# Kernel optimization log

Hardware: AMD Instinct MI355X
Metric: run time of the kernel (lower is better)

## Reference

```python
import jax, jax.numpy as jnp
import numpy as np

EMBED_DIM = 256
N_COMP = 50
SIGMA_INIT = 1.0
EPS = 1e-8


def setup_inputs() -> dict:
    key = jax.random.key(0)
    ks = jax.random.split(key, 9)
    B, N, D, C = 1, 8192, EMBED_DIM, N_COMP
    s = 0.05
    return {
        "embeddings": jax.random.normal(ks[0], (B, N, D), dtype=jnp.float32),
        # trajectory_projection: Linear(D, D//2) -> GELU -> (Dropout, eval) -> Linear(D//2, D//4) -> GELU -> Linear(D//4, C)
        "W1": jax.random.normal(ks[1], (D, D // 2), dtype=jnp.float32) * s,
        "b1": jnp.zeros((D // 2,), dtype=jnp.float32),
        "W2": jax.random.normal(ks[2], (D // 2, D // 4), dtype=jnp.float32) * s,
        "b2": jnp.zeros((D // 4,), dtype=jnp.float32),
        "W3": jax.random.normal(ks[3], (D // 4, C), dtype=jnp.float32) * s,
        "b3": jnp.zeros((C,), dtype=jnp.float32),
        "diffusion_weights": jax.random.normal(ks[4], (C,), dtype=jnp.float32),
        "adaptive_sigma": jnp.asarray(SIGMA_INIT, dtype=jnp.float32),
    }


def reference(embeddings, W1, b1, W2, b2, W3, b3, diffusion_weights, adaptive_sigma):
    B, N, D = embeddings.shape
    # trajectory projection (dropout is identity in eval mode); torch GELU default is exact (erf)
    h = jax.nn.gelu(embeddings @ W1 + b1, approximate=False)
    h = jax.nn.gelu(h @ W2 + b2, approximate=False)
    coords = h @ W3 + b3  # [B, N, C]

    # gaussian kernel: pairwise squared distances via sum-of-squares GEMM trick
    sq = jnp.sum(coords * coords, axis=-1)  # [B, N]
    d2 = sq[:, :, None] + sq[:, None, :] - 2.0 * jnp.einsum("bnc,bmc->bnm", coords, coords)
    d2 = jnp.maximum(d2, 0.0)
    sig = jnp.clip(adaptive_sigma, 0.1, 10.0)
    kernel = jnp.exp(-d2 / (2.0 * sig * sig))  # [B, N, N]

    # diffusion weights: softmax over n_components, tiled up to n_cells
    w = jax.nn.softmax(diffusion_weights, axis=0)  # [C]
    C = w.shape[0]
    repeat_factor = (N + C - 1) // C
    w_full = jnp.tile(w, repeat_factor)[:N]  # [N]

    weighted = kernel * w_full[None, None, :]
    row_sums = jnp.sum(weighted, axis=-1, keepdims=True)
    transition = weighted / (row_sums + EPS)
    return transition
```

## Files before the change

### kernel.cpp

```cpp
#include <hip/hip_runtime.h>
#include <hip/hip_bf16.h>

#define NTOK 8192
#define KP   64
#define EPSV 1e-8f

typedef __attribute__((ext_vector_type(4))) float f32x4;
typedef __attribute__((ext_vector_type(8))) short bf16x8;

__global__ __launch_bounds__(256) void k_mlp(
    const float* __restrict__ emb,
    const float* __restrict__ W1, const float* __restrict__ b1,
    const float* __restrict__ W2, const float* __restrict__ b2,
    const float* __restrict__ W3, const float* __restrict__ b3,
    __hip_bfloat16* __restrict__ coordsb, float* __restrict__ sqg)
{
    __shared__ float E[32 * 256];
    __shared__ float H1[32 * 128];
    __shared__ float H2[32 * 64];
    __shared__ float C3[32 * 50];

    const int tid  = threadIdx.x;
    const int brow = blockIdx.x * 32;

    {
        const float4* src = (const float4*)(emb + (size_t)brow * 256);
        float4* dst = (float4*)E;
        for (int i = tid; i < 32 * 256 / 4; i += 256) dst[i] = src[i];
    }
    __syncthreads();

    {
        const int j = tid & 127, rh = tid >> 7;
        float acc[16];
        const float bb = b1[j];
        #pragma unroll
        for (int r = 0; r < 16; ++r) acc[r] = bb;
        for (int k = 0; k < 256; k += 4) {
            const float w0 = W1[(k + 0) * 128 + j];
            const float w1 = W1[(k + 1) * 128 + j];
            const float w2 = W1[(k + 2) * 128 + j];
            const float w3 = W1[(k + 3) * 128 + j];
            #pragma unroll
            for (int r = 0; r < 16; ++r) {
                const float4 e = *(const float4*)&E[(rh * 16 + r) * 256 + k];
                acc[r] = fmaf(e.x, w0, acc[r]);
                acc[r] = fmaf(e.y, w1, acc[r]);
                acc[r] = fmaf(e.z, w2, acc[r]);
                acc[r] = fmaf(e.w, w3, acc[r]);
            }
        }
        #pragma unroll
        for (int r = 0; r < 16; ++r) {
            const float h = acc[r];
            H1[(rh * 16 + r) * 128 + j] = 0.5f * h * (1.0f + erff(h * 0.70710678118654752f));
        }
    }
    __syncthreads();

    {
        const int j = tid & 63, rg = tid >> 6;
        float acc[8];
        const float bb = b2[j];
        #pragma unroll
        for (int r = 0; r < 8; ++r) acc[r] = bb;
        for (int k = 0; k < 128; k += 4) {
            const float w0 = W2[(k + 0) * 64 + j];
            const float w1 = W2[(k + 1) * 64 + j];
            const float w2v = W2[(k + 2) * 64 + j];
            const float w3v = W2[(k + 3) * 64 + j];
            #pragma unroll
            for (int r = 0; r < 8; ++r) {
                const float4 h = *(const float4*)&H1[(rg * 8 + r) * 128 + k];
                acc[r] = fmaf(h.x, w0, acc[r]);
                acc[r] = fmaf(h.y, w1, acc[r]);
                acc[r] = fmaf(h.z, w2v, acc[r]);
                acc[r] = fmaf(h.w, w3v, acc[r]);
            }
        }
        #pragma unroll
        for (int r = 0; r < 8; ++r) {
            const float h = acc[r];
            H2[(rg * 8 + r) * 64 + j] = 0.5f * h * (1.0f + erff(h * 0.70710678118654752f));
        }
    }
    __syncthreads();

    for (int o = tid; o < 32 * 50; o += 256) {
        const int r = o / 50;
        const int c = o - r * 50;
        float acc = b3[c];
        for (int k = 0; k < 64; k += 4) {
            const float4 h = *(const float4*)&H2[r * 64 + k];
            acc = fmaf(h.x, W3[(k + 0) * 50 + c], acc);
            acc = fmaf(h.y, W3[(k + 1) * 50 + c], acc);
            acc = fmaf(h.z, W3[(k + 2) * 50 + c], acc);
            acc = fmaf(h.w, W3[(k + 3) * 50 + c], acc);
        }
        C3[o] = acc;
    }
    __syncthreads();

    if (tid < 32) {
        float s = 0.0f;
        for (int c = 0; c < 50; ++c) { const float v = C3[tid * 50 + c]; s = fmaf(v, v, s); }
        sqg[brow + tid] = s;
    }
    for (int i = tid; i < 32 * KP; i += 256) {
        const int r = i >> 6, c = i & 63;
        const float v = (c < 50) ? C3[r * 50 + c] : 0.0f;
        coordsb[(size_t)(brow + r) * KP + c] = __float2bfloat16(v);
    }
}

__global__ __launch_bounds__(256) void k_wfull(
    const float* __restrict__ dw, float* __restrict__ wfull, float* __restrict__ rowsum)
{
    __shared__ float w[50];
    const int tid = threadIdx.x;
    if (tid < 50) w[tid] = dw[tid];
    __syncthreads();
    float m = -1e30f;
    for (int i = 0; i < 50; ++i) m = fmaxf(m, w[i]);
    float s = 0.0f;
    for (int i = 0; i < 50; ++i) s += __expf(w[i] - m);
    const float inv = 1.0f / s;
    const int i = blockIdx.x * 256 + tid;
    const int c = i % 50;
    wfull[i]  = __expf(w[c] - m) * inv;
    rowsum[i] = 0.0f;
}

__global__ __launch_bounds__(256) void k_rowsum(
    const unsigned short* __restrict__ Xb, const float* __restrict__ sqg,
    const float* __restrict__ wfull, const float* __restrict__ sigp,
    float* __restrict__ rowsum)
{
    const int tid  = threadIdx.x;
    const int lane = tid & 63;
    const int wv   = tid >> 6;
    const int r0   = blockIdx.x * 64 + wv * 16;
    const int m0   = blockIdx.y * 1024;
    const int lr   = lane & 15;
    const int lk   = lane >> 4;

    const float sg    = fminf(fmaxf(sigp[0], 0.1f), 10.0f);
    const float scale = -1.4426950408889634f / (2.0f * sg * sg);

    const bf16x8 a0 = *(const bf16x8*)(Xb + (size_t)(r0 + lr) * KP + 0 * 32 + lk * 8);
    const bf16x8 a1 = *(const bf16x8*)(Xb + (size_t)(r0 + lr) * KP + 1 * 32 + lk * 8);
    float sqn[4];
    #pragma unroll
    for (int j = 0; j < 4; ++j) sqn[j] = sqg[r0 + lk * 4 + j];

    float rs[4] = {0.f, 0.f, 0.f, 0.f};
    for (int mt = m0; mt < m0 + 1024; mt += 16) {
        const bf16x8 bA = *(const bf16x8*)(Xb + (size_t)(mt + lr) * KP + 0 * 32 + lk * 8);
        const bf16x8 bB = *(const bf16x8*)(Xb + (size_t)(mt + lr) * KP + 1 * 32 + lk * 8);
        f32x4 acc = {0.f, 0.f, 0.f, 0.f};
        acc = __builtin_amdgcn_mfma_f32_16x16x32_bf16(a0, bA, acc, 0, 0, 0);
        acc = __builtin_amdgcn_mfma_f32_16x16x32_bf16(a1, bB, acc, 0, 0, 0);
        const float sqm = sqg[mt + lr];
        const float wm  = wfull[mt + lr];
        #pragma unroll
        for (int j = 0; j < 4; ++j) {
            const float d2 = fmaxf(sqn[j] + sqm - 2.0f * acc[j], 0.0f);
            rs[j] += exp2f(d2 * scale) * wm;
        }
    }
    #pragma unroll
    for (int j = 0; j < 4; ++j) {
        float v = rs[j];
        v += __shfl_xor(v, 1);
        v += __shfl_xor(v, 2);
        v += __shfl_xor(v, 4);
        v += __shfl_xor(v, 8);
        if (lr == 0) atomicAdd(&rowsum[r0 + lk * 4 + j], v);
    }
}

__global__ __launch_bounds__(256) void k_out(
    const unsigned short* __restrict__ Xb, const float* __restrict__ sqg,
    const float* __restrict__ wfull, const float* __restrict__ sigp,
    const float* __restrict__ rowsum, float* __restrict__ out)
{
    const int tid  = threadIdx.x;
    const int lane = tid & 63;
    const int wv   = tid >> 6;
    const int n0   = blockIdx.x * 64 + wv * 16;
    const int m0   = blockIdx.y * 1024;
    const int lr   = lane & 15;
    const int lk   = lane >> 4;

    const float sg    = fminf(fmaxf(sigp[0], 0.1f), 10.0f);
    const float scale = -1.4426950408889634f / (2.0f * sg * sg);

    const bf16x8 b0 = *(const bf16x8*)(Xb + (size_t)(n0 + lr) * KP + 0 * 32 + lk * 8);
    const bf16x8 b1 = *(const bf16x8*)(Xb + (size_t)(n0 + lr) * KP + 1 * 32 + lk * 8);
    const float sqn_l = sqg[n0 + lr];
    const float inv_l = 1.0f / (rowsum[n0 + lr] + EPSV);

    for (int mt = m0; mt < m0 + 1024; mt += 16) {
        const bf16x8 aA = *(const bf16x8*)(Xb + (size_t)(mt + lr) * KP + 0 * 32 + lk * 8);
        const bf16x8 aB = *(const bf16x8*)(Xb + (size_t)(mt + lr) * KP + 1 * 32 + lk * 8);
        f32x4 acc = {0.f, 0.f, 0.f, 0.f};
        acc = __builtin_amdgcn_mfma_f32_16x16x32_bf16(aA, b0, acc, 0, 0, 0);
        acc = __builtin_amdgcn_mfma_f32_16x16x32_bf16(aB, b1, acc, 0, 0, 0);

        const float4 sqm4 = *(const float4*)&sqg[mt + lk * 4];
        const float4 wm4  = *(const float4*)&wfull[mt + lk * 4];

        float4 o;
        {
            const float d2x = fmaxf(sqn_l + sqm4.x - 2.0f * acc[0], 0.0f);
            const float d2y = fmaxf(sqn_l + sqm4.y - 2.0f * acc[1], 0.0f);
            const float d2z = fmaxf(sqn_l + sqm4.z - 2.0f * acc[2], 0.0f);
            const float d2w = fmaxf(sqn_l + sqm4.w - 2.0f * acc[3], 0.0f);
            o.x = exp2f(d2x * scale) * wm4.x * inv_l;
            o.y = exp2f(d2y * scale) * wm4.y * inv_l;
            o.z = exp2f(d2z * scale) * wm4.z * inv_l;
            o.w = exp2f(d2w * scale) * wm4.w * inv_l;
        }
        *(float4*)&out[(size_t)(n0 + lr) * NTOK + mt + lk * 4] = o;
    }
}

extern "C" void kernel_launch(void* const* d_in, const int* in_sizes, int n_in,
                              void* d_out, int out_size, void* d_ws, size_t ws_size,
                              hipStream_t stream)
{
    const float* emb = (const float*)d_in[0];
    const float* W1  = (const float*)d_in[1];
    const float* b1  = (const float*)d_in[2];
    const float* W2  = (const float*)d_in[3];
    const float* b2  = (const float*)d_in[4];
    const float* W3  = (const float*)d_in[5];
    const float* b3  = (const float*)d_in[6];
    const float* dw  = (const float*)d_in[7];
    const float* sig = (const float*)d_in[8];
    float* out = (float*)d_out;

    char* ws = (char*)d_ws;
    __hip_bfloat16* coordsb = (__hip_bfloat16*)ws;
    float* sqg    = (float*)(ws + 1048576);
    float* wfull  = (float*)(ws + 1048576 + 32768);
    float* rowsum = (float*)(ws + 1048576 + 65536);

    hipLaunchKernelGGL(k_mlp, dim3(NTOK / 32), dim3(256), 0, stream,
                       emb, W1, b1, W2, b2, W3, b3, coordsb, sqg);
    hipLaunchKernelGGL(k_wfull, dim3(NTOK / 256), dim3(256), 0, stream, dw, wfull, rowsum);
    hipLaunchKernelGGL(k_rowsum, dim3(NTOK / 64, 8), dim3(256), 0, stream,
                       (const unsigned short*)coordsb, sqg, wfull, sig, rowsum);
    hipLaunchKernelGGL(k_out, dim3(NTOK / 64, 8), dim3(256), 0, stream,
                       (const unsigned short*)coordsb, sqg, wfull, sig, rowsum, out);
}
```

Before: 475.9 us.

## Halve MLP tile rows, unroll kernel loops, use raw exp2 and nontemporal stores

```diff
diff --git a/kernel.cpp b/kernel.cpp
--- a/kernel.cpp
+++ b/kernel.cpp
@@ -7,6 +7,12 @@
 
 typedef __attribute__((ext_vector_type(4))) float f32x4;
 typedef __attribute__((ext_vector_type(8))) short bf16x8;
+
+__device__ __forceinline__ float fexp2(float x) {
+    float r;
+    asm("v_exp_f32 %0, %1" : "=v"(r) : "v"(x));
+    return r;
+}
 
 __global__ __launch_bounds__(256) void k_mlp(
     const float* __restrict__ emb,
@@ -15,35 +21,36 @@
     const float* __restrict__ W3, const float* __restrict__ b3,
     __hip_bfloat16* __restrict__ coordsb, float* __restrict__ sqg)
 {
-    __shared__ float E[32 * 256];
-    __shared__ float H1[32 * 128];
-    __shared__ float H2[32 * 64];
-    __shared__ float C3[32 * 50];
+    __shared__ float E[16 * 256];
+    __shared__ float H1[16 * 128];
+    __shared__ float H2[16 * 64];
+    __shared__ float C3[16 * 50];
 
     const int tid  = threadIdx.x;
-    const int brow = blockIdx.x * 32;
+    const int brow = blockIdx.x * 16;
 
     {
         const float4* src = (const float4*)(emb + (size_t)brow * 256);
         float4* dst = (float4*)E;
-        for (int i = tid; i < 32 * 256 / 4; i += 256) dst[i] = src[i];
+        #pragma unroll
+        for (int i = 0; i < 4; ++i) dst[tid + i * 256] = src[tid + i * 256];
     }
     __syncthreads();
 
     {
         const int j = tid & 127, rh = tid >> 7;
-        float acc[16];
+        float acc[8];
         const float bb = b1[j];
         #pragma unroll
-        for (int r = 0; r < 16; ++r) acc[r] = bb;
+        for (int r = 0; r < 8; ++r) acc[r] = bb;
         for (int k = 0; k < 256; k += 4) {
             const float w0 = W1[(k + 0) * 128 + j];
             const float w1 = W1[(k + 1) * 128 + j];
             const float w2 = W1[(k + 2) * 128 + j];
             const float w3 = W1[(k + 3) * 128 + j];
             #pragma unroll
-            for (int r = 0; r < 16; ++r) {
-                const float4 e = *(const float4*)&E[(rh * 16 + r) * 256 + k];
+            for (int r = 0; r < 8; ++r) {
+                const float4 e = *(const float4*)&E[(rh * 8 + r) * 256 + k];
                 acc[r] = fmaf(e.x, w0, acc[r]);
                 acc[r] = fmaf(e.y, w1, acc[r]);
                 acc[r] = fmaf(e.z, w2, acc[r]);
@@ -51,27 +58,27 @@
             }
         }
         #pragma unroll
-        for (int r = 0; r < 16; ++r) {
+        for (int r = 0; r < 8; ++r) {
             const float h = acc[r];
-            H1[(rh * 16 + r) * 128 + j] = 0.5f * h * (1.0f + erff(h * 0.70710678118654752f));
+            H1[(rh * 8 + r) * 128 + j] = 0.5f * h * (1.0f + erff(h * 0.70710678118654752f));
         }
     }
     __syncthreads();
 
     {
         const int j = tid & 63, rg = tid >> 6;
-        float acc[8];
+        float acc[4];
         const float bb = b2[j];
         #pragma unroll
-        for (int r = 0; r < 8; ++r) acc[r] = bb;
+        for (int r = 0; r < 4; ++r) acc[r] = bb;
         for (int k = 0; k < 128; k += 4) {
             const float w0 = W2[(k + 0) * 64 + j];
             const float w1 = W2[(k + 1) * 64 + j];
             const float w2v = W2[(k + 2) * 64 + j];
             const float w3v = W2[(k + 3) * 64 + j];
             #pragma unroll
-            for (int r = 0; r < 8; ++r) {
-                const float4 h = *(const float4*)&H1[(rg * 8 + r) * 128 + k];
+            for (int r = 0; r < 4; ++r) {
+                const float4 h = *(const float4*)&H1[(rg * 4 + r) * 128 + k];
                 acc[r] = fmaf(h.x, w0, acc[r]);
                 acc[r] = fmaf(h.y, w1, acc[r]);
                 acc[r] = fmaf(h.z, w2v, acc[r]);
@@ -79,14 +86,14 @@
             }
         }
         #pragma unroll
-        for (int r = 0; r < 8; ++r) {
+        for (int r = 0; r < 4; ++r) {
             const float h = acc[r];
-            H2[(rg * 8 + r) * 64 + j] = 0.5f * h * (1.0f + erff(h * 0.70710678118654752f));
-        }
-    }
-    __syncthreads();
-
-    for (int o = tid; o < 32 * 50; o += 256) {
+            H2[(rg * 4 + r) * 64 + j] = 0.5f * h * (1.0f + erff(h * 0.70710678118654752f));
+        }
+    }
+    __syncthreads();
+
+    for (int o = tid; o < 16 * 50; o += 256) {
         const int r = o / 50;
         const int c = o - r * 50;
         float acc = b3[c];
@@ -101,12 +108,14 @@
     }
     __syncthreads();
 
-    if (tid < 32) {
+    if (tid < 16) {
         float s = 0.0f;
         for (int c = 0; c < 50; ++c) { const float v = C3[tid * 50 + c]; s = fmaf(v, v, s); }
         sqg[brow + tid] = s;
     }
-    for (int i = tid; i < 32 * KP; i += 256) {
+    #pragma unroll
+    for (int ii = 0; ii < 4; ++ii) {
+        const int i = tid + ii * 256;
         const int r = i >> 6, c = i & 63;
         const float v = (c < 50) ? C3[r * 50 + c] : 0.0f;
         coordsb[(size_t)(brow + r) * KP + c] = __float2bfloat16(v);
@@ -131,7 +140,7 @@
     rowsum[i] = 0.0f;
 }
 
-__global__ __launch_bounds__(256) void k_rowsum(
+__global__ __launch_bounds__(256, 4) void k_rowsum(
     const unsigned short* __restrict__ Xb, const float* __restrict__ sqg,
     const float* __restrict__ wfull, const float* __restrict__ sigp,
     float* __restrict__ rowsum)
@@ -146,26 +155,39 @@
 
     const float sg    = fminf(fmaxf(sigp[0], 0.1f), 10.0f);
     const float scale = -1.4426950408889634f / (2.0f * sg * sg);
+    const float m2s   = -2.0f * scale;
 
     const bf16x8 a0 = *(const bf16x8*)(Xb + (size_t)(r0 + lr) * KP + 0 * 32 + lk * 8);
     const bf16x8 a1 = *(const bf16x8*)(Xb + (size_t)(r0 + lr) * KP + 1 * 32 + lk * 8);
-    float sqn[4];
+    float sqnS[4];
     #pragma unroll
-    for (int j = 0; j < 4; ++j) sqn[j] = sqg[r0 + lk * 4 + j];
+    for (int j = 0; j < 4; ++j) sqnS[j] = sqg[r0 + lk * 4 + j] * scale;
 
     float rs[4] = {0.f, 0.f, 0.f, 0.f};
-    for (int mt = m0; mt < m0 + 1024; mt += 16) {
-        const bf16x8 bA = *(const bf16x8*)(Xb + (size_t)(mt + lr) * KP + 0 * 32 + lk * 8);
-        const bf16x8 bB = *(const bf16x8*)(Xb + (size_t)(mt + lr) * KP + 1 * 32 + lk * 8);
-        f32x4 acc = {0.f, 0.f, 0.f, 0.f};
-        acc = __builtin_amdgcn_mfma_f32_16x16x32_bf16(a0, bA, acc, 0, 0, 0);
-        acc = __builtin_amdgcn_mfma_f32_16x16x32_bf16(a1, bB, acc, 0, 0, 0);
-        const float sqm = sqg[mt + lr];
-        const float wm  = wfull[mt + lr];
-        #pragma unroll
-        for (int j = 0; j < 4; ++j) {
-            const float d2 = fmaxf(sqn[j] + sqm - 2.0f * acc[j], 0.0f);
-            rs[j] += exp2f(d2 * scale) * wm;
+    for (int mt = m0; mt < m0 + 1024; mt += 32) {
+        bf16x8 bA[2], bB[2];
+        #pragma unroll
+        for (int t = 0; t < 2; ++t) {
+            bA[t] = *(const bf16x8*)(Xb + (size_t)(mt + t * 16 + lr) * KP + 0 * 32 + lk * 8);
+            bB[t] = *(const bf16x8*)(Xb + (size_t)(mt + t * 16 + lr) * KP + 1 * 32 + lk * 8);
+        }
+        f32x4 acc[2];
+        #pragma unroll
+        for (int t = 0; t < 2; ++t) {
+            f32x4 z = {0.f, 0.f, 0.f, 0.f};
+            z = __builtin_amdgcn_mfma_f32_16x16x32_bf16(a0, bA[t], z, 0, 0, 0);
+            z = __builtin_amdgcn_mfma_f32_16x16x32_bf16(a1, bB[t], z, 0, 0, 0);
+            acc[t] = z;
+        }
+        #pragma unroll
+        for (int t = 0; t < 2; ++t) {
+            const float sqmS = sqg[mt + t * 16 + lr] * scale;
+            const float wm   = wfull[mt + t * 16 + lr];
+            #pragma unroll
+            for (int j = 0; j < 4; ++j) {
+                const float tt = fmaf(m2s, acc[t][j], sqnS[j] + sqmS);
+                rs[j] = fmaf(fexp2(fminf(tt, 0.0f)), wm, rs[j]);
+            }
         }
     }
     #pragma unroll
@@ -179,7 +201,7 @@
     }
 }
 
-__global__ __launch_bounds__(256) void k_out(
+__global__ __launch_bounds__(256, 4) void k_out(
     const unsigned short* __restrict__ Xb, const float* __restrict__ sqg,
     const float* __restrict__ wfull, const float* __restrict__ sigp,
     const float* __restrict__ rowsum, float* __restrict__ out)
@@ -194,34 +216,40 @@
 
     const float sg    = fminf(fmaxf(sigp[0], 0.1f), 10.0f);
     const float scale = -1.4426950408889634f / (2.0f * sg * sg);
+    const float m2s   = -2.0f * scale;
 
     const bf16x8 b0 = *(const bf16x8*)(Xb + (size_t)(n0 + lr) * KP + 0 * 32 + lk * 8);
     const bf16x8 b1 = *(const bf16x8*)(Xb + (size_t)(n0 + lr) * KP + 1 * 32 + lk * 8);
-    const float sqn_l = sqg[n0 + lr];
+    const float sqnS  = sqg[n0 + lr] * scale;
     const float inv_l = 1.0f / (rowsum[n0 + lr] + EPSV);
-
-    for (int mt = m0; mt < m0 + 1024; mt += 16) {
-        const bf16x8 aA = *(const bf16x8*)(Xb + (size_t)(mt + lr) * KP + 0 * 32 + lk * 8);
-        const bf16x8 aB = *(const bf16x8*)(Xb + (size_t)(mt + lr) * KP + 1 * 32 + lk * 8);
-        f32x4 acc = {0.f, 0.f, 0.f, 0.f};
-        acc = __builtin_amdgcn_mfma_f32_16x16x32_bf16(aA, b0, acc, 0, 0, 0);
-        acc = __builtin_amdgcn_mfma_f32_16x16x32_bf16(aB, b1, acc, 0, 0, 0);
-
-        const float4 sqm4 = *(const float4*)&sqg[mt + lk * 4];
-        const float4 wm4  = *(const float4*)&wfull[mt + lk * 4];
-
-        float4 o;
-        {
-            const float d2x = fmaxf(sqn_l + sqm4.x - 2.0f * acc[0], 0.0f);
-            const float d2y = fmaxf(sqn_l + sqm4.y - 2.0f * acc[1], 0.0f);
-            const float d2z = fmaxf(sqn_l + sqm4.z - 2.0f * acc[2], 0.0f);
-            const float d2w = fmaxf(sqn_l + sqm4.w - 2.0f * acc[3], 0.0f);
-            o.x = exp2f(d2x * scale) * wm4.x * inv_l;
-            o.y = exp2f(d2y * scale) * wm4.y * inv_l;
-            o.z = exp2f(d2z * scale) * wm4.z * inv_l;
-            o.w = exp2f(d2w * scale) * wm4.w * inv_l;
-        }
-        *(float4*)&out[(size_t)(n0 + lr) * NTOK + mt + lk * 4] = o;
+    float* const orow = out + (size_t)(n0 + lr) * NTOK;
+
+    for (int mt = m0; mt < m0 + 1024; mt += 32) {
+        bf16x8 aA[2], aB[2];
+        #pragma unroll
+        for (int t = 0; t < 2; ++t) {
+            aA[t] = *(const bf16x8*)(Xb + (size_t)(mt + t * 16 + lr) * KP + 0 * 32 + lk * 8);
+            aB[t] = *(const bf16x8*)(Xb + (size_t)(mt + t * 16 + lr) * KP + 1 * 32 + lk * 8);
+        }
+        f32x4 acc[2];
+        #pragma unroll
+        for (int t = 0; t < 2; ++t) {
+            f32x4 z = {0.f, 0.f, 0.f, 0.f};
+            z = __builtin_amdgcn_mfma_f32_16x16x32_bf16(aA[t], b0, z, 0, 0, 0);
+            z = __builtin_amdgcn_mfma_f32_16x16x32_bf16(aB[t], b1, z, 0, 0, 0);
+            acc[t] = z;
+        }
+        #pragma unroll
+        for (int t = 0; t < 2; ++t) {
+            const float4 sqm4 = *(const float4*)&sqg[mt + t * 16 + lk * 4];
+            const float4 wm4  = *(const float4*)&wfull[mt + t * 16 + lk * 4];
+            f32x4 o;
+            o[0] = fexp2(fminf(fmaf(m2s, acc[t][0], fmaf(sqm4.x, scale, sqnS)), 0.0f)) * wm4.x * inv_l;
+            o[1] = fexp2(fminf(fmaf(m2s, acc[t][1], fmaf(sqm4.y, scale, sqnS)), 0.0f)) * wm4.y * inv_l;
+            o[2] = fexp2(fminf(fmaf(m2s, acc[t][2], fmaf(sqm4.z, scale, sqnS)), 0.0f)) * wm4.z * inv_l;
+            o[3] = fexp2(fminf(fmaf(m2s, acc[t][3], fmaf(sqm4.w, scale, sqnS)), 0.0f)) * wm4.w * inv_l;
+            __builtin_nontemporal_store(o, (f32x4*)&orow[mt + t * 16 + lk * 4]);
+        }
     }
 }
 
@@ -246,7 +274,7 @@
     float* wfull  = (float*)(ws + 1048576 + 32768);
     float* rowsum = (float*)(ws + 1048576 + 65536);
 
-    hipLaunchKernelGGL(k_mlp, dim3(NTOK / 32), dim3(256), 0, stream,
+    hipLaunchKernelGGL(k_mlp, dim3(NTOK / 16), dim3(256), 0, stream,
                        emb, W1, b1, W2, b2, W3, b3, coordsb, sqg);
     hipLaunchKernelGGL(k_wfull, dim3(NTOK / 256), dim3(256), 0, stream, dw, wfull, rowsum);
     hipLaunchKernelGGL(k_rowsum, dim3(NTOK / 64, 8), dim3(256), 0, stream,
```

New measurement: 520.5 us. 9.4% more time.
